# Kernel optimization log

Measured on AMD Instinct MI355X. Metric: run time of the kernel, lower is better.

The kernel has to match this reference:

```python
import jax, jax.numpy as jnp
import numpy as np
from jax import lax

IN_FEATURES = 1024
HIDDEN = 1024
N_LEAVES = 2048
STACK_DEPTH = 4  # comb tree never exceeds stack depth 2


def _make_ops(n_leaves):
    # left-leaning comb tree: shift shift reduce, then (shift reduce)*
    ops = [0, 0, 1] + [0, 1] * (n_leaves - 2)
    return jnp.asarray(np.array(ops, dtype=np.int32))


def _xavier(key, shape):
    fan_in, fan_out = shape[1], shape[0]
    bound = np.sqrt(6.0 / (fan_in + fan_out)).astype(np.float32)
    return jax.random.uniform(key, shape, jnp.float32, -bound, bound)


def setup_inputs() -> dict:
    key = jax.random.key(0)
    k = jax.random.split(key, 4)
    n_nodes = 2 * N_LEAVES - 1
    xs = jax.random.normal(k[0], (n_nodes, IN_FEATURES), jnp.float32)
    ops = _make_ops(N_LEAVES)
    W_ih = _xavier(k[1], (5 * HIDDEN, IN_FEATURES))
    W_lhh = _xavier(k[2], (5 * HIDDEN, HIDDEN))
    W_rhh = _xavier(k[3], (5 * HIDDEN, HIDDEN))
    # biases: zeros except forget-gate slices [H:3H] set to 1 (per reset_parameters)
    b = jnp.zeros((5 * HIDDEN,), jnp.float32).at[HIDDEN:3 * HIDDEN].set(1.0)
    return {"xs": xs, "ops": ops, "W_ih": W_ih, "W_lhh": W_lhh, "W_rhh": W_rhh,
            "b_ih": b, "b_lhh": b, "b_rhh": b}


def _tree_lstm(xs, ops, W_ih, W_lhh, W_rhh, b_ih, b_lhh, b_rhh):
    H = W_lhh.shape[1]
    # hoist the input projection out of the serial scan: [N, 5H]
    ih_all = xs @ W_ih.T + (b_ih + b_lhh + b_rhh)

    def step(carry, inp):
        stack_h, stack_c, ptr = carry  # stack_*: [D, H], ptr: int32 stack size
        ih_t, op = inp
        is_red = op == 1
        ridx = jnp.clip(ptr - 1, 0, STACK_DEPTH - 1)
        lidx = jnp.clip(ptr - 2, 0, STACK_DEPTH - 1)
        zero = jnp.zeros((H,), stack_h.dtype)
        rh = jnp.where(is_red, stack_h[ridx], zero)
        rc = jnp.where(is_red, stack_c[ridx], zero)
        lh = jnp.where(is_red, stack_h[lidx], zero)
        lc = jnp.where(is_red, stack_c[lidx], zero)
        gates = ih_t + lh @ W_lhh.T + rh @ W_rhh.T  # [5H]
        i, lf, rf, g, o = jnp.split(gates, 5)
        i = jax.nn.sigmoid(i)
        lf = jax.nn.sigmoid(lf)
        rf = jax.nn.sigmoid(rf)
        g = jnp.tanh(g)
        o = jax.nn.sigmoid(o)
        yc = lf * lc + rf * rc + i * g
        yh = o * jnp.tanh(yc)
        pos = jnp.where(is_red, ptr - 2, ptr)  # reduce pops 2 then pushes 1
        stack_h = lax.dynamic_update_slice(stack_h, yh[None, :], (pos, 0))
        stack_c = lax.dynamic_update_slice(stack_c, yc[None, :], (pos, 0))
        return (stack_h, stack_c, pos + 1), (yh, yc)

    carry0 = (jnp.zeros((STACK_DEPTH, H), xs.dtype),
              jnp.zeros((STACK_DEPTH, H), xs.dtype),
              jnp.int32(0))
    _, (hs, cs) = lax.scan(step, carry0, (ih_all, ops))
    root_h = hs[-1]  # last produced state is the root (stack ends with size 1)
    return root_h, hs, cs


def reference(xs, ops, W_ih, W_lhh, W_rhh, b_ih, b_lhh, b_rhh):
    return _tree_lstm(xs, ops, W_ih, W_lhh, W_rhh, b_ih, b_lhh, b_rhh)
```

## Files before the change

kernel.cpp:

```cpp
#include <hip/hip_runtime.h>
#include <hip/hip_bf16.h>
#include <stdint.h>

#define HDIM 1024
#define GDIM 5120
#define NWG_SER 128
#define RPW 10
#define NAN_U 0x7FC00000u

typedef __attribute__((ext_vector_type(8))) short v8s;
typedef __attribute__((ext_vector_type(4))) float v4f;

constexpr long long PRE_OFF   = 0;
constexpr long long LEAFG_OFF = PRE_OFF   + 2048LL * 5120 * 4;
constexpr long long DUMP_OFF  = LEAFG_OFF + 2048LL * 5120 * 4;
constexpr long long XSBF_OFF  = DUMP_OFF  + 8192LL * 4;
constexpr long long WIH_OFF   = XSBF_OFF  + 4096LL * 1024 * 2;
constexpr long long WLHH_OFF  = WIH_OFF   + 5120LL * 1024 * 2;
constexpr long long WRHH_OFF  = WLHH_OFF  + 5120LL * 1024 * 2;
constexpr long long HBF_OFF   = WRHH_OFF  + 5120LL * 1024 * 2;
constexpr long long B3_OFF    = HBF_OFF   + 4096LL * 1024 * 2;
constexpr long long PLAN_OFF  = B3_OFF    + 5120LL * 4;

constexpr int P_TRED = 0, P_LNODE = 2048, P_RNODE = 4096, P_FLAGS = 6144,
              P_TLEAF = 8192, P_DEST1 = 10240, P_NODER = 14336, P_DESTR = 16384,
              P_NODEL = 18432, P_DESTL = 20480, P_CNT = 22528;

constexpr int PRE_E   = 0;
constexpr int LEAFG_E = (int)(LEAFG_OFF / 4);
constexpr int DUMP_E  = (int)(DUMP_OFF / 4);

static __device__ __forceinline__ float sigf(float x) { return 1.0f / (1.0f + __expf(-x)); }
static __device__ __forceinline__ float tanh_f(float x) {
  if (x > 15.0f) return 1.0f;
  if (x < -15.0f) return -1.0f;
  float e = __expf(2.0f * x);
  return (e - 1.0f) / (e + 1.0f);
}
static __device__ __forceinline__ unsigned short f2bf(float x) {
  __hip_bfloat16 h = __float2bfloat16(x);
  union { __hip_bfloat16 h; unsigned short u; } cv;
  cv.h = h;
  return cv.u;
}

__global__ void plan_kernel(const int* __restrict__ ops, int n_nodes, int* __restrict__ plan) {
  __shared__ int sops[4096];
  for (int i = threadIdx.x; i < n_nodes; i += 256) sops[i] = ops[i];
  __syncthreads();
  if (threadIdx.x != 0) return;
  int stack[4] = {0, 0, 0, 0};
  int ptr = 0, nred = 0, nleaf = 0, nR = 0, nL = 0;
  for (int t = 0; t < n_nodes; ++t) {
    int op = sops[t];
    if (op == 1) {
      int ridx = min(max(ptr - 1, 0), 3);
      int lidx = min(max(ptr - 2, 0), 3);
      int ln = stack[lidx], rn = stack[ridx];
      int r = nred++;
      plan[P_TRED + r] = t;
      plan[P_LNODE + r] = ln;
      plan[P_RNODE + r] = rn;
      int pos = min(max(ptr - 2, 0), 3);
      int lred = (sops[ln] == 1) ? 1 : 0;
      int rred = (sops[rn] == 1) ? 2 : 0;
      plan[P_FLAGS + r] = lred | rred | (lidx << 2) | (ridx << 4) | (pos << 6);
      plan[P_DEST1 + t] = PRE_E + r * GDIM;
      if (!rred) { plan[P_NODER + nR] = rn; plan[P_DESTR + nR] = PRE_E + r * GDIM; nR++; }
      if (!lred) { plan[P_NODEL + nL] = ln; plan[P_DESTL + nL] = PRE_E + r * GDIM; nL++; }
      stack[pos] = t;
      ptr = (ptr - 2) + 1;
    } else {
      int li = nleaf++;
      plan[P_TLEAF + li] = t;
      plan[P_DEST1 + t] = LEAFG_E + li * GDIM;
      stack[min(max(ptr, 0), 3)] = t;
      ptr = ptr + 1;
    }
  }
  for (int i = n_nodes; i < 4096; ++i) plan[P_DEST1 + i] = DUMP_E;
  for (int i = nR; i < 2048; ++i) { plan[P_NODER + i] = 0; plan[P_DESTR + i] = DUMP_E; }
  for (int i = nL; i < 2048; ++i) { plan[P_NODEL + i] = 0; plan[P_DESTL + i] = DUMP_E; }
  plan[P_CNT + 0] = nred;
  plan[P_CNT + 1] = nR;
  plan[P_CNT + 2] = nL;
  plan[P_CNT + 3] = n_nodes;
}

__global__ void init_nan_kernel(const int* __restrict__ ops, int n_nodes,
                                unsigned int* __restrict__ hsu) {
  const int t = blockIdx.x;
  if (t >= n_nodes || ops[t] != 1) return;
  uint4 nv = make_uint4(NAN_U, NAN_U, NAN_U, NAN_U);
  *(uint4*)(hsu + (long long)t * HDIM + threadIdx.x * 4) = nv;
}

__global__ void cvt_bf16_kernel(const float* __restrict__ src, unsigned short* __restrict__ dst,
                                int ntotal, int nsrc) {
  int i = (blockIdx.x * 256 + threadIdx.x) * 4;
  if (i >= ntotal) return;
  float4 v = make_float4(0.f, 0.f, 0.f, 0.f);
  if (i < nsrc) v = *(const float4*)(src + i);
  ushort4 o;
  o.x = f2bf(v.x); o.y = f2bf(v.y); o.z = f2bf(v.z); o.w = f2bf(v.w);
  *(ushort4*)(dst + i) = o;
}

__global__ void b3_kernel(const float* __restrict__ a, const float* __restrict__ b,
                          const float* __restrict__ c, float* __restrict__ o) {
  int i = blockIdx.x * 256 + threadIdx.x;
  if (i < GDIM) o[i] = a[i] + b[i] + c[i];
}

template <int GATHER, int ACCUM>
__global__ __launch_bounds__(256, 1) void gemm_bt(
    const unsigned short* __restrict__ A, const unsigned short* __restrict__ B,
    const int* __restrict__ gidx, const int* __restrict__ dest,
    float* __restrict__ wsf, const float* __restrict__ b3,
    const int* __restrict__ activeRows) {
  if ((int)blockIdx.x * 128 >= *activeRows) return;
  __shared__ unsigned short As[128 * 32];
  __shared__ unsigned short Bs[128 * 32];
  const int tid = threadIdx.x;
  const int w = tid >> 6, l = tid & 63;
  const int tm = blockIdx.x, tn = blockIdx.y;
  const int q0 = w * 2, q1 = w * 2 + 1;
  const int r0 = q0 * 16 + (l >> 2), r1 = q1 * 16 + (l >> 2);
  const int ck = (l & 3) * 8;
  int ga0 = tm * 128 + r0, ga1 = tm * 128 + r1;
  if (GATHER) { ga0 = gidx[ga0]; ga1 = gidx[ga1]; }
  const unsigned short* ap0 = A + (long long)ga0 * HDIM + ck;
  const unsigned short* ap1 = A + (long long)ga1 * HDIM + ck;
  const unsigned short* bp0 = B + (long long)(tn * 128 + r0) * HDIM + ck;
  const unsigned short* bp1 = B + (long long)(tn * 128 + r1) * HDIM + ck;
  uint4* asd0 = (uint4*)(As + q0 * 512) + l;
  uint4* asd1 = (uint4*)(As + q1 * 512) + l;
  uint4* bsd0 = (uint4*)(Bs + q0 * 512) + l;
  uint4* bsd1 = (uint4*)(Bs + q1 * 512) + l;
  const int wr = w >> 1, wc = w & 1;
  const int lrow = l & 15, lq = l >> 4;
  const unsigned short* Ard = As + (wr * 64 + lrow) * 32 + lq * 8;
  const unsigned short* Brd = Bs + (wc * 64 + lrow) * 32 + lq * 8;
  v4f acc[4][4];
#pragma unroll
  for (int m = 0; m < 4; ++m)
#pragma unroll
    for (int n = 0; n < 4; ++n) acc[m][n] = (v4f){0.f, 0.f, 0.f, 0.f};
  for (int kb = 0; kb < 32; ++kb) {
    const int ko = kb * 32;
    uint4 a0 = *(const uint4*)(ap0 + ko);
    uint4 a1 = *(const uint4*)(ap1 + ko);
    uint4 b0 = *(const uint4*)(bp0 + ko);
    uint4 b1 = *(const uint4*)(bp1 + ko);
    __syncthreads();
    *asd0 = a0; *asd1 = a1; *bsd0 = b0; *bsd1 = b1;
    __syncthreads();
    v8s af[4], bfr[4];
#pragma unroll
    for (int m = 0; m < 4; ++m) af[m] = *(const v8s*)(Ard + m * 512);
#pragma unroll
    for (int n = 0; n < 4; ++n) bfr[n] = *(const v8s*)(Brd + n * 512);
#pragma unroll
    for (int m = 0; m < 4; ++m)
#pragma unroll
      for (int n = 0; n < 4; ++n)
        acc[m][n] = __builtin_amdgcn_mfma_f32_16x16x32_bf16(af[m], bfr[n], acc[m][n], 0, 0, 0);
  }
#pragma unroll
  for (int m = 0; m < 4; ++m) {
#pragma unroll
    for (int jj = 0; jj < 4; ++jj) {
      const int arow = tm * 128 + wr * 64 + m * 16 + lq * 4 + jj;
      const int doff = dest[arow];
#pragma unroll
      for (int n = 0; n < 4; ++n) {
        const int col = tn * 128 + wc * 64 + n * 16 + lrow;
        float v = acc[m][n][jj];
        if (ACCUM) wsf[doff + col] += v;
        else wsf[doff + col] = v + b3[col];
      }
    }
  }
}

__global__ void leaf_cell(const float* __restrict__ leafg, const int* __restrict__ plan,
                          float* __restrict__ hs, float* __restrict__ cs,
                          unsigned short* __restrict__ hbf) {
  const int li = blockIdx.x;
  const int j = threadIdx.x * 4;
  const float* row = leafg + (long long)li * GDIM;
  float4 gi = *(const float4*)(row + j);
  float4 gg = *(const float4*)(row + 3 * HDIM + j);
  float4 go = *(const float4*)(row + 4 * HDIM + j);
  const int t = plan[P_TLEAF + li];
  float4 yc, yh;
  yc.x = sigf(gi.x) * tanh_f(gg.x); yc.y = sigf(gi.y) * tanh_f(gg.y);
  yc.z = sigf(gi.z) * tanh_f(gg.z); yc.w = sigf(gi.w) * tanh_f(gg.w);
  yh.x = sigf(go.x) * tanh_f(yc.x); yh.y = sigf(go.y) * tanh_f(yc.y);
  yh.z = sigf(go.z) * tanh_f(yc.z); yh.w = sigf(go.w) * tanh_f(yc.w);
  *(float4*)(hs + (long long)t * HDIM + j) = yh;
  *(float4*)(cs + (long long)t * HDIM + j) = yc;
  ushort4 hb;
  hb.x = f2bf(yh.x); hb.y = f2bf(yh.y); hb.z = f2bf(yh.z); hb.w = f2bf(yh.w);
  *(ushort4*)(hbf + (long long)t * HDIM + j) = hb;
}

__global__ __launch_bounds__(256, 1) void serial_chain(
    const float* __restrict__ Wl, const float* __restrict__ Wr,
    const float* __restrict__ pre, const int* __restrict__ plan,
    float* __restrict__ hs, float* __restrict__ cs) {
  const int wg = blockIdx.x;
  const int tid = threadIdx.x;
  const int w = tid >> 6, l = tid & 63;
  __shared__ int s_t[2048], s_ln[2048], s_rn[2048], s_fl[2048];
  __shared__ float gsum[40];
  __shared__ float c_stack[4][8];
  const int nred = plan[P_CNT + 0];
  for (int i = tid; i < nred; i += 256) {
    s_t[i] = plan[P_TRED + i];
    s_ln[i] = plan[P_LNODE + i];
    s_rn[i] = plan[P_RNODE + i];
    s_fl[i] = plan[P_FLAGS + i];
  }
  float wreg[RPW][16];
#pragma unroll
  for (int rr = 0; rr < RPW; ++rr) {
    const int ridx = w * RPW + rr;
    const long long row = (long long)((ridx >> 3) * HDIM + wg * 8 + (ridx & 7)) * HDIM;
#pragma unroll
    for (int q = 0; q < 16; ++q) wreg[rr][q] = Wl[row + q * 64 + l];
  }
  float pv0 = 0.f, pv1 = 0.f, pv2 = 0.f, pv3 = 0.f, pv4 = 0.f;
  if (tid < 8) {
    const float* pr = pre + wg * 8 + tid;
    pv0 = pr[0]; pv1 = pr[HDIM]; pv2 = pr[2 * HDIM]; pv3 = pr[3 * HDIM]; pv4 = pr[4 * HDIM];
  }
  __syncthreads();
  for (int r = 0; r < nred; ++r) {
    const int t = s_t[r], ln = s_ln[r], rn = s_rn[r], fl = s_fl[r];
    float lc = 0.f, rc = 0.f;
    if (tid < 8) {
      const int jj = wg * 8 + tid;
      if (fl & 1) lc = c_stack[(fl >> 2) & 3][tid];
      else        lc = cs[(long long)ln * HDIM + jj];
      if (fl & 2) rc = c_stack[(fl >> 4) & 3][tid];
      else        rc = cs[(long long)rn * HDIM + jj];
    }
    float hv[16];
    {
      const float* hrow = hs + (long long)ln * HDIM;
      if (fl & 1) {
        bool ready = false;
        while (!ready) {
          ready = true;
#pragma unroll
          for (int q = 0; q < 16; ++q) {
            unsigned int u = __hip_atomic_load((unsigned int*)(hrow + q * 64 + l),
                                               __ATOMIC_RELAXED, __HIP_MEMORY_SCOPE_AGENT);
            ready = ready && (u != NAN_U);
            hv[q] = __uint_as_float(u);
          }
        }
      } else {
#pragma unroll
        for (int q = 0; q < 16; ++q) hv[q] = hrow[q * 64 + l];
      }
    }
    float acc[RPW];
#pragma unroll
    for (int rr = 0; rr < RPW; ++rr) acc[rr] = 0.f;
#pragma unroll
    for (int rr = 0; rr < RPW; ++rr)
#pragma unroll
      for (int q = 0; q < 16; ++q) acc[rr] = fmaf(wreg[rr][q], hv[q], acc[rr]);
    if (fl & 2) {
      float hv2[16];
      const float* hrow2 = hs + (long long)rn * HDIM;
      bool ready = false;
      while (!ready) {
        ready = true;
#pragma unroll
        for (int q = 0; q < 16; ++q) {
          unsigned int u = __hip_atomic_load((unsigned int*)(hrow2 + q * 64 + l),
                                             __ATOMIC_RELAXED, __HIP_MEMORY_SCOPE_AGENT);
          ready = ready && (u != NAN_U);
          hv2[q] = __uint_as_float(u);
        }
      }
#pragma unroll
      for (int rr = 0; rr < RPW; ++rr) {
        const int ridx = w * RPW + rr;
        const long long row = (long long)((ridx >> 3) * HDIM + wg * 8 + (ridx & 7)) * HDIM;
#pragma unroll
        for (int q = 0; q < 16; ++q) acc[rr] = fmaf(Wr[row + q * 64 + l], hv2[q], acc[rr]);
      }
    }
#pragma unroll
    for (int rr = 0; rr < RPW; ++rr) {
      float v = acc[rr];
      v += __shfl_xor(v, 32); v += __shfl_xor(v, 16); v += __shfl_xor(v, 8);
      v += __shfl_xor(v, 4);  v += __shfl_xor(v, 2);  v += __shfl_xor(v, 1);
      if (l == 0) gsum[w * RPW + rr] = v;
    }
    __syncthreads();
    if (tid < 8) {
      const int jj = wg * 8 + tid;
      const float xi  = pv0 + gsum[0 * 8 + tid];
      const float xlf = pv1 + gsum[1 * 8 + tid];
      const float xrf = pv2 + gsum[2 * 8 + tid];
      const float xg  = pv3 + gsum[3 * 8 + tid];
      const float xo  = pv4 + gsum[4 * 8 + tid];
      const float ii = sigf(xi), lf = sigf(xlf), rf = sigf(xrf);
      const float gv = tanh_f(xg), oo = sigf(xo);
      const float yc = lf * lc + rf * rc + ii * gv;
      const float yh = oo * tanh_f(yc);
      cs[(long long)t * HDIM + jj] = yc;
      c_stack[(fl >> 6) & 3][tid] = yc;
      __hip_atomic_store((unsigned int*)&hs[(long long)t * HDIM + jj], __float_as_uint(yh),
                         __ATOMIC_RELAXED, __HIP_MEMORY_SCOPE_AGENT);
      if (r + 1 < nred) {
        const float* pr = pre + (long long)(r + 1) * GDIM + jj;
        pv0 = pr[0]; pv1 = pr[HDIM]; pv2 = pr[2 * HDIM]; pv3 = pr[3 * HDIM]; pv4 = pr[4 * HDIM];
      }
    }
    __syncthreads();
  }
}

__global__ void root_copy(float* __restrict__ out, const float* __restrict__ hs, int n_nodes) {
  int j = blockIdx.x * 256 + threadIdx.x;
  if (j < HDIM) out[j] = hs[(long long)(n_nodes - 1) * HDIM + j];
}

extern "C" void kernel_launch(void* const* d_in, const int* in_sizes, int n_in,
                              void* d_out, int out_size, void* d_ws, size_t ws_size,
                              hipStream_t stream) {
  const float* xs = (const float*)d_in[0];
  const int* ops = (const int*)d_in[1];
  const float* Wih = (const float*)d_in[2];
  const float* Wlhh = (const float*)d_in[3];
  const float* Wrhh = (const float*)d_in[4];
  const float* bih = (const float*)d_in[5];
  const float* blhh = (const float*)d_in[6];
  const float* brhh = (const float*)d_in[7];
  const int n_nodes = in_sizes[0] / HDIM;

  char* ws = (char*)d_ws;
  float* wsf = (float*)d_ws;
  float* pre = (float*)(ws + PRE_OFF);
  float* leafg = (float*)(ws + LEAFG_OFF);
  unsigned short* xsbf = (unsigned short*)(ws + XSBF_OFF);
  unsigned short* wihb = (unsigned short*)(ws + WIH_OFF);
  unsigned short* wlhb = (unsigned short*)(ws + WLHH_OFF);
  unsigned short* wrhb = (unsigned short*)(ws + WRHH_OFF);
  unsigned short* hbf = (unsigned short*)(ws + HBF_OFF);
  float* b3 = (float*)(ws + B3_OFF);
  int* plan = (int*)(ws + PLAN_OFF);

  float* out = (float*)d_out;
  float* hs = out + HDIM;
  float* cs = hs + (long long)n_nodes * HDIM;

  hipLaunchKernelGGL(plan_kernel, dim3(1), dim3(256), 0, stream, ops, n_nodes, plan);
  hipLaunchKernelGGL(init_nan_kernel, dim3(n_nodes), dim3(256), 0, stream,
                     ops, n_nodes, (unsigned int*)hs);
  hipLaunchKernelGGL(cvt_bf16_kernel, dim3(4096), dim3(256), 0, stream,
                     xs, xsbf, 4096 * HDIM, n_nodes * HDIM);
  hipLaunchKernelGGL(cvt_bf16_kernel, dim3(5120), dim3(256), 0, stream,
                     Wih, wihb, GDIM * HDIM, GDIM * HDIM);
  hipLaunchKernelGGL(cvt_bf16_kernel, dim3(5120), dim3(256), 0, stream,
                     Wlhh, wlhb, GDIM * HDIM, GDIM * HDIM);
  hipLaunchKernelGGL(cvt_bf16_kernel, dim3(5120), dim3(256), 0, stream,
                     Wrhh, wrhb, GDIM * HDIM, GDIM * HDIM);
  hipLaunchKernelGGL(b3_kernel, dim3(20), dim3(256), 0, stream, bih, blhh, brhh, b3);
  hipLaunchKernelGGL((gemm_bt<0, 0>), dim3(32, 40), dim3(256), 0, stream,
                     xsbf, wihb, (const int*)nullptr, plan + P_DEST1, wsf, b3, plan + P_CNT + 3);
  hipLaunchKernelGGL(leaf_cell, dim3((n_nodes + 1) / 2), dim3(256), 0, stream,
                     leafg, plan, hs, cs, hbf);
  hipLaunchKernelGGL((gemm_bt<1, 1>), dim3(16, 40), dim3(256), 0, stream,
                     hbf, wrhb, plan + P_NODER, plan + P_DESTR, wsf, (const float*)nullptr, plan + P_CNT + 1);
  hipLaunchKernelGGL((gemm_bt<1, 1>), dim3(16, 40), dim3(256), 0, stream,
                     hbf, wlhb, plan + P_NODEL, plan + P_DESTL, wsf, (const float*)nullptr, plan + P_CNT + 2);
  hipLaunchKernelGGL(serial_chain, dim3(NWG_SER), dim3(256), 0, stream,
                     Wlhh, Wrhh, pre, plan, hs, cs);
  hipLaunchKernelGGL(root_copy, dim3(4), dim3(256), 0, stream, out, hs, n_nodes);
}
```

Measured before the change: 9.616 ms.

## Halve serial-chain workgroups and stage polled h vectors in LDS

The serial recurrence kernel now runs 64 workgroups of 512 threads, each covering 16 hidden units instead of 8. That halves the number of workgroups polling global memory for each new hidden state. Polling is also reduced: only one wavefront polls the left child's h and another polls the right child's, using 64-bit atomic loads, and they share the values through LDS with an extra barrier. This cuts redundant cross-workgroup spin traffic at the cost of an added __syncthreads per step and more register pressure from the launch bound of 2.

```diff
diff --git a/kernel.cpp b/kernel.cpp
--- a/kernel.cpp
+++ b/kernel.cpp
@@ -4,7 +4,8 @@
 
 #define HDIM 1024
 #define GDIM 5120
-#define NWG_SER 128
+#define NWG_SER 64
+#define TPB_SER 512
 #define RPW 10
 #define NAN_U 0x7FC00000u
 
@@ -205,7 +206,7 @@
   *(ushort4*)(hbf + (long long)t * HDIM + j) = hb;
 }
 
-__global__ __launch_bounds__(256, 1) void serial_chain(
+__global__ __launch_bounds__(TPB_SER, 2) void serial_chain(
     const float* __restrict__ Wl, const float* __restrict__ Wr,
     const float* __restrict__ pre, const int* __restrict__ plan,
     float* __restrict__ hs, float* __restrict__ cs) {
@@ -213,10 +214,12 @@
   const int tid = threadIdx.x;
   const int w = tid >> 6, l = tid & 63;
   __shared__ int s_t[2048], s_ln[2048], s_rn[2048], s_fl[2048];
-  __shared__ float gsum[40];
-  __shared__ float c_stack[4][8];
+  __shared__ float h_sh[1024];
+  __shared__ float h_sh2[1024];
+  __shared__ float gsum[80];
+  __shared__ float c_stack[4][16];
   const int nred = plan[P_CNT + 0];
-  for (int i = tid; i < nred; i += 256) {
+  for (int i = tid; i < nred; i += TPB_SER) {
     s_t[i] = plan[P_TRED + i];
     s_ln[i] = plan[P_LNODE + i];
     s_rn[i] = plan[P_RNODE + i];
@@ -226,46 +229,77 @@
 #pragma unroll
   for (int rr = 0; rr < RPW; ++rr) {
     const int ridx = w * RPW + rr;
-    const long long row = (long long)((ridx >> 3) * HDIM + wg * 8 + (ridx & 7)) * HDIM;
+    const long long row = (long long)((ridx >> 4) * HDIM + wg * 16 + (ridx & 15)) * HDIM;
 #pragma unroll
     for (int q = 0; q < 16; ++q) wreg[rr][q] = Wl[row + q * 64 + l];
   }
   float pv0 = 0.f, pv1 = 0.f, pv2 = 0.f, pv3 = 0.f, pv4 = 0.f;
-  if (tid < 8) {
-    const float* pr = pre + wg * 8 + tid;
+  if (tid < 16) {
+    const float* pr = pre + wg * 16 + tid;
     pv0 = pr[0]; pv1 = pr[HDIM]; pv2 = pr[2 * HDIM]; pv3 = pr[3 * HDIM]; pv4 = pr[4 * HDIM];
   }
   __syncthreads();
   for (int r = 0; r < nred; ++r) {
     const int t = s_t[r], ln = s_ln[r], rn = s_rn[r], fl = s_fl[r];
     float lc = 0.f, rc = 0.f;
-    if (tid < 8) {
-      const int jj = wg * 8 + tid;
+    if (tid < 16) {
+      const int jj = wg * 16 + tid;
       if (fl & 1) lc = c_stack[(fl >> 2) & 3][tid];
       else        lc = cs[(long long)ln * HDIM + jj];
       if (fl & 2) rc = c_stack[(fl >> 4) & 3][tid];
       else        rc = cs[(long long)rn * HDIM + jj];
     }
-    float hv[16];
-    {
-      const float* hrow = hs + (long long)ln * HDIM;
+    if (w == 0) {
+      const unsigned long long* hrow = (const unsigned long long*)(hs + (long long)ln * HDIM);
+      unsigned long long hv64[8];
       if (fl & 1) {
         bool ready = false;
         while (!ready) {
           ready = true;
 #pragma unroll
-          for (int q = 0; q < 16; ++q) {
-            unsigned int u = __hip_atomic_load((unsigned int*)(hrow + q * 64 + l),
-                                               __ATOMIC_RELAXED, __HIP_MEMORY_SCOPE_AGENT);
-            ready = ready && (u != NAN_U);
-            hv[q] = __uint_as_float(u);
+          for (int p = 0; p < 8; ++p) {
+            unsigned long long u = __hip_atomic_load(hrow + p * 64 + l,
+                                                     __ATOMIC_RELAXED, __HIP_MEMORY_SCOPE_AGENT);
+            ready = ready && ((unsigned int)u != NAN_U) && ((unsigned int)(u >> 32) != NAN_U);
+            hv64[p] = u;
           }
         }
       } else {
 #pragma unroll
-        for (int q = 0; q < 16; ++q) hv[q] = hrow[q * 64 + l];
-      }
-    }
+        for (int p = 0; p < 8; ++p) hv64[p] = hrow[p * 64 + l];
+      }
+#pragma unroll
+      for (int p = 0; p < 8; ++p) {
+        const int c = (p * 64 + l) * 2;
+        h_sh[c] = __uint_as_float((unsigned int)hv64[p]);
+        h_sh[c + 1] = __uint_as_float((unsigned int)(hv64[p] >> 32));
+      }
+    }
+    if ((fl & 2) && w == 1) {
+      const unsigned long long* hrow = (const unsigned long long*)(hs + (long long)rn * HDIM);
+      unsigned long long hv64[8];
+      bool ready = false;
+      while (!ready) {
+        ready = true;
+#pragma unroll
+        for (int p = 0; p < 8; ++p) {
+          unsigned long long u = __hip_atomic_load(hrow + p * 64 + l,
+                                                   __ATOMIC_RELAXED, __HIP_MEMORY_SCOPE_AGENT);
+          ready = ready && ((unsigned int)u != NAN_U) && ((unsigned int)(u >> 32) != NAN_U);
+          hv64[p] = u;
+        }
+      }
+#pragma unroll
+      for (int p = 0; p < 8; ++p) {
+        const int c = (p * 64 + l) * 2;
+        h_sh2[c] = __uint_as_float((unsigned int)hv64[p]);
+        h_sh2[c + 1] = __uint_as_float((unsigned int)(hv64[p] >> 32));
+      }
+    }
+    __syncthreads();
+    float hv[16];
+#pragma unroll
+    for (int q = 0; q < 16; ++q) hv[q] = h_sh[q * 64 + l];
     float acc[RPW];
 #pragma unroll
     for (int rr = 0; rr < RPW; ++rr) acc[rr] = 0.f;
@@ -275,22 +309,12 @@
       for (int q = 0; q < 16; ++q) acc[rr] = fmaf(wreg[rr][q], hv[q], acc[rr]);
     if (fl & 2) {
       float hv2[16];
-      const float* hrow2 = hs + (long long)rn * HDIM;
-      bool ready = false;
-      while (!ready) {
-        ready = true;
-#pragma unroll
-        for (int q = 0; q < 16; ++q) {
-          unsigned int u = __hip_atomic_load((unsigned int*)(hrow2 + q * 64 + l),
-                                             __ATOMIC_RELAXED, __HIP_MEMORY_SCOPE_AGENT);
-          ready = ready && (u != NAN_U);
-          hv2[q] = __uint_as_float(u);
-        }
-      }
+#pragma unroll
+      for (int q = 0; q < 16; ++q) hv2[q] = h_sh2[q * 64 + l];
 #pragma unroll
       for (int rr = 0; rr < RPW; ++rr) {
         const int ridx = w * RPW + rr;
-        const long long row = (long long)((ridx >> 3) * HDIM + wg * 8 + (ridx & 7)) * HDIM;
+        const long long row = (long long)((ridx >> 4) * HDIM + wg * 16 + (ridx & 15)) * HDIM;
 #pragma unroll
         for (int q = 0; q < 16; ++q) acc[rr] = fmaf(Wr[row + q * 64 + l], hv2[q], acc[rr]);
       }
@@ -303,13 +327,13 @@
       if (l == 0) gsum[w * RPW + rr] = v;
     }
     __syncthreads();
-    if (tid < 8) {
-      const int jj = wg * 8 + tid;
-      const float xi  = pv0 + gsum[0 * 8 + tid];
-      const float xlf = pv1 + gsum[1 * 8 + tid];
-      const float xrf = pv2 + gsum[2 * 8 + tid];
-      const float xg  = pv3 + gsum[3 * 8 + tid];
-      const float xo  = pv4 + gsum[4 * 8 + tid];
+    if (tid < 16) {
+      const int jj = wg * 16 + tid;
+      const float xi  = pv0 + gsum[0 * 16 + tid];
+      const float xlf = pv1 + gsum[1 * 16 + tid];
+      const float xrf = pv2 + gsum[2 * 16 + tid];
+      const float xg  = pv3 + gsum[3 * 16 + tid];
+      const float xo  = pv4 + gsum[4 * 16 + tid];
       const float ii = sigf(xi), lf = sigf(xlf), rf = sigf(xrf);
       const float gv = tanh_f(xg), oo = sigf(xo);
       const float yc = lf * lc + rf * rc + ii * gv;
@@ -381,7 +405,7 @@
                      hbf, wrhb, plan + P_NODER, plan + P_DESTR, wsf, (const float*)nullptr, plan + P_CNT + 1);
   hipLaunchKernelGGL((gemm_bt<1, 1>), dim3(16, 40), dim3(256), 0, stream,
                      hbf, wlhb, plan + P_NODEL, plan + P_DESTL, wsf, (const float*)nullptr, plan + P_CNT + 2);
-  hipLaunchKernelGGL(serial_chain, dim3(NWG_SER), dim3(256), 0, stream,
+  hipLaunchKernelGGL(serial_chain, dim3(NWG_SER), dim3(TPB_SER), 0, stream,
                      Wlhh, Wrhh, pre, plan, hs, cs);
   hipLaunchKernelGGL(root_copy, dim3(4), dim3(256), 0, stream, out, hs, n_nodes);
 }
```

New measurement: 11.57 ms. 1.2x slower.

## Make serial chain waves independent with per-wave channel ownership and ready flags

Applied to the files above, without the earlier changes.

Each wave in the serial recurrence kernel now owns two hidden channels and computes all five gates for them. The gate reduction and cell update stay inside the wave, which removes the two block-wide barriers and the LDS gate exchange on every step. A per-wave byte-flag window in workspace is polled before the NaN-sentinel check on dependent hidden rows, with s_sleep backoff in the spin loops. In exchange the flags are never reset, so they only gate correctly within the first window and otherwise rely on the NaN polling. Each wave also re-reads Wr rows directly and issues more small global loads per step.

```diff
diff --git a/kernel.cpp b/kernel.cpp
--- a/kernel.cpp
+++ b/kernel.cpp
@@ -5,8 +5,9 @@
 #define HDIM 1024
 #define GDIM 5120
 #define NWG_SER 128
-#define RPW 10
+#define TPB_SER 256
 #define NAN_U 0x7FC00000u
+#define FLAG_WIN 64
 
 typedef __attribute__((ext_vector_type(8))) short v8s;
 typedef __attribute__((ext_vector_type(4))) float v4f;
@@ -21,10 +22,12 @@
 constexpr long long HBF_OFF   = WRHH_OFF  + 5120LL * 1024 * 2;
 constexpr long long B3_OFF    = HBF_OFF   + 4096LL * 1024 * 2;
 constexpr long long PLAN_OFF  = B3_OFF    + 5120LL * 4;
+constexpr long long FLAG_OFF  = PLAN_OFF  + 26688LL * 4;
 
 constexpr int P_TRED = 0, P_LNODE = 2048, P_RNODE = 4096, P_FLAGS = 6144,
               P_TLEAF = 8192, P_DEST1 = 10240, P_NODER = 14336, P_DESTR = 16384,
-              P_NODEL = 18432, P_DESTL = 20480, P_CNT = 22528;
+              P_NODEL = 18432, P_DESTL = 20480, P_CNT = 22528,
+              P_LRX = 22592, P_RRX = 24640;
 
 constexpr int PRE_E   = 0;
 constexpr int LEAFG_E = (int)(LEAFG_OFF / 4);
@@ -46,6 +49,7 @@
 
 __global__ void plan_kernel(const int* __restrict__ ops, int n_nodes, int* __restrict__ plan) {
   __shared__ int sops[4096];
+  __shared__ int red_of[4096];
   for (int i = threadIdx.x; i < n_nodes; i += 256) sops[i] = ops[i];
   __syncthreads();
   if (threadIdx.x != 0) return;
@@ -65,9 +69,12 @@
       int lred = (sops[ln] == 1) ? 1 : 0;
       int rred = (sops[rn] == 1) ? 2 : 0;
       plan[P_FLAGS + r] = lred | rred | (lidx << 2) | (ridx << 4) | (pos << 6);
+      plan[P_LRX + r] = lred ? red_of[ln] : 0;
+      plan[P_RRX + r] = rred ? red_of[rn] : 0;
       plan[P_DEST1 + t] = PRE_E + r * GDIM;
       if (!rred) { plan[P_NODER + nR] = rn; plan[P_DESTR + nR] = PRE_E + r * GDIM; nR++; }
       if (!lred) { plan[P_NODEL + nL] = ln; plan[P_DESTL + nL] = PRE_E + r * GDIM; nL++; }
+      red_of[t] = r;
       stack[pos] = t;
       ptr = (ptr - 2) + 1;
     } else {
@@ -205,125 +212,163 @@
   *(ushort4*)(hbf + (long long)t * HDIM + j) = hb;
 }
 
-__global__ __launch_bounds__(256, 1) void serial_chain(
+__global__ __launch_bounds__(TPB_SER, 1) void serial_chain(
     const float* __restrict__ Wl, const float* __restrict__ Wr,
     const float* __restrict__ pre, const int* __restrict__ plan,
-    float* __restrict__ hs, float* __restrict__ cs) {
+    float* __restrict__ hs, float* __restrict__ cs,
+    unsigned char* __restrict__ flags) {
   const int wg = blockIdx.x;
   const int tid = threadIdx.x;
   const int w = tid >> 6, l = tid & 63;
-  __shared__ int s_t[2048], s_ln[2048], s_rn[2048], s_fl[2048];
-  __shared__ float gsum[40];
-  __shared__ float c_stack[4][8];
+  const int wid = wg * 4 + w;
+  const int ch0 = wid * 2;
+  __shared__ int s_t[2048], s_ln[2048], s_rn[2048], s_fl[2048], s_lrx[2048], s_rrx[2048];
   const int nred = plan[P_CNT + 0];
-  for (int i = tid; i < nred; i += 256) {
+  for (int i = tid; i < nred; i += TPB_SER) {
     s_t[i] = plan[P_TRED + i];
     s_ln[i] = plan[P_LNODE + i];
     s_rn[i] = plan[P_RNODE + i];
     s_fl[i] = plan[P_FLAGS + i];
+    s_lrx[i] = plan[P_LRX + i];
+    s_rrx[i] = plan[P_RRX + i];
   }
-  float wreg[RPW][16];
-#pragma unroll
-  for (int rr = 0; rr < RPW; ++rr) {
-    const int ridx = w * RPW + rr;
-    const long long row = (long long)((ridx >> 3) * HDIM + wg * 8 + (ridx & 7)) * HDIM;
-#pragma unroll
-    for (int q = 0; q < 16; ++q) wreg[rr][q] = Wl[row + q * 64 + l];
-  }
-  float pv0 = 0.f, pv1 = 0.f, pv2 = 0.f, pv3 = 0.f, pv4 = 0.f;
-  if (tid < 8) {
-    const float* pr = pre + wg * 8 + tid;
-    pv0 = pr[0]; pv1 = pr[HDIM]; pv2 = pr[2 * HDIM]; pv3 = pr[3 * HDIM]; pv4 = pr[4 * HDIM];
-  }
+  float wreg[10][16];
+#pragma unroll
+  for (int c = 0; c < 2; ++c)
+#pragma unroll
+    for (int g = 0; g < 5; ++g) {
+      const float* wp = Wl + (long long)(g * HDIM + ch0 + c) * HDIM + l;
+#pragma unroll
+      for (int q = 0; q < 16; ++q) wreg[c * 5 + g][q] = wp[q * 64];
+    }
+  float cst0 = 0.f, cst1 = 0.f, cst2 = 0.f, cst3 = 0.f;
   __syncthreads();
+  unsigned int* fu = (unsigned int*)flags;
   for (int r = 0; r < nred; ++r) {
     const int t = s_t[r], ln = s_ln[r], rn = s_rn[r], fl = s_fl[r];
-    float lc = 0.f, rc = 0.f;
-    if (tid < 8) {
-      const int jj = wg * 8 + tid;
-      if (fl & 1) lc = c_stack[(fl >> 2) & 3][tid];
-      else        lc = cs[(long long)ln * HDIM + jj];
-      if (fl & 2) rc = c_stack[(fl >> 4) & 3][tid];
-      else        rc = cs[(long long)rn * HDIM + jj];
+    float pv0 = 0.f, pv1 = 0.f, pv2 = 0.f, pv3 = 0.f, pv4 = 0.f, lcv = 0.f, rcv = 0.f;
+    if (l < 2) {
+      const float* pr = pre + (long long)r * GDIM + ch0 + l;
+      pv0 = pr[0]; pv1 = pr[HDIM]; pv2 = pr[2 * HDIM]; pv3 = pr[3 * HDIM]; pv4 = pr[4 * HDIM];
+      if (!(fl & 1)) lcv = cs[(long long)ln * HDIM + ch0 + l];
+      if (!(fl & 2)) rcv = cs[(long long)rn * HDIM + ch0 + l];
+    }
+    {
+      const int lidx = (fl >> 2) & 3, ridx = (fl >> 4) & 3;
+      const float lst = (lidx == 0) ? cst0 : (lidx == 1) ? cst1 : (lidx == 2) ? cst2 : cst3;
+      const float rst = (ridx == 0) ? cst0 : (ridx == 1) ? cst1 : (ridx == 2) ? cst2 : cst3;
+      if (fl & 1) lcv = lst;
+      if (fl & 2) rcv = rst;
+    }
+    if (fl & 1) {
+      const unsigned int* fwp = fu + (unsigned)((s_lrx[r] & (FLAG_WIN - 1)) * 128);
+      for (;;) {
+        unsigned int d0 = __hip_atomic_load(fwp + l, __ATOMIC_RELAXED, __HIP_MEMORY_SCOPE_AGENT);
+        unsigned int d1 = __hip_atomic_load(fwp + 64 + l, __ATOMIC_RELAXED, __HIP_MEMORY_SCOPE_AGENT);
+        if (__all((d0 == 0x01010101u) && (d1 == 0x01010101u))) break;
+        __builtin_amdgcn_s_sleep(1);
+      }
     }
     float hv[16];
     {
       const float* hrow = hs + (long long)ln * HDIM;
       if (fl & 1) {
-        bool ready = false;
-        while (!ready) {
-          ready = true;
+        for (;;) {
+          bool ready = true;
 #pragma unroll
           for (int q = 0; q < 16; ++q) {
-            unsigned int u = __hip_atomic_load((unsigned int*)(hrow + q * 64 + l),
+            unsigned int u = __hip_atomic_load((const unsigned int*)(hrow + q * 64 + l),
                                                __ATOMIC_RELAXED, __HIP_MEMORY_SCOPE_AGENT);
             ready = ready && (u != NAN_U);
             hv[q] = __uint_as_float(u);
           }
+          if (__all(ready)) break;
+          __builtin_amdgcn_s_sleep(1);
         }
       } else {
 #pragma unroll
         for (int q = 0; q < 16; ++q) hv[q] = hrow[q * 64 + l];
       }
     }
-    float acc[RPW];
-#pragma unroll
-    for (int rr = 0; rr < RPW; ++rr) acc[rr] = 0.f;
-#pragma unroll
-    for (int rr = 0; rr < RPW; ++rr)
-#pragma unroll
-      for (int q = 0; q < 16; ++q) acc[rr] = fmaf(wreg[rr][q], hv[q], acc[rr]);
+    float acc[10];
+#pragma unroll
+    for (int k = 0; k < 10; ++k) acc[k] = 0.f;
+#pragma unroll
+    for (int k = 0; k < 10; ++k)
+#pragma unroll
+      for (int q = 0; q < 16; ++q) acc[k] = fmaf(wreg[k][q], hv[q], acc[k]);
     if (fl & 2) {
+      const unsigned int* fwp = fu + (unsigned)((s_rrx[r] & (FLAG_WIN - 1)) * 128);
+      for (;;) {
+        unsigned int d0 = __hip_atomic_load(fwp + l, __ATOMIC_RELAXED, __HIP_MEMORY_SCOPE_AGENT);
+        unsigned int d1 = __hip_atomic_load(fwp + 64 + l, __ATOMIC_RELAXED, __HIP_MEMORY_SCOPE_AGENT);
+        if (__all((d0 == 0x01010101u) && (d1 == 0x01010101u))) break;
+        __builtin_amdgcn_s_sleep(1);
+      }
       float hv2[16];
       const float* hrow2 = hs + (long long)rn * HDIM;
-      bool ready = false;
-      while (!ready) {
-        ready = true;
+      for (;;) {
+        bool ready = true;
 #pragma unroll
         for (int q = 0; q < 16; ++q) {
-          unsigned int u = __hip_atomic_load((unsigned int*)(hrow2 + q * 64 + l),
+          unsigned int u = __hip_atomic_load((const unsigned int*)(hrow2 + q * 64 + l),
                                              __ATOMIC_RELAXED, __HIP_MEMORY_SCOPE_AGENT);
           ready = ready && (u != NAN_U);
           hv2[q] = __uint_as_float(u);
         }
+        if (__all(ready)) break;
+        __builtin_amdgcn_s_sleep(1);
       }
 #pragma unroll
-      for (int rr = 0; rr < RPW; ++rr) {
-        const int ridx = w * RPW + rr;
-        const long long row = (long long)((ridx >> 3) * HDIM + wg * 8 + (ridx & 7)) * HDIM;
-#pragma unroll
-        for (int q = 0; q < 16; ++q) acc[rr] = fmaf(Wr[row + q * 64 + l], hv2[q], acc[rr]);
-      }
-    }
-#pragma unroll
-    for (int rr = 0; rr < RPW; ++rr) {
-      float v = acc[rr];
+      for (int c = 0; c < 2; ++c)
+#pragma unroll
+        for (int g = 0; g < 5; ++g) {
+          const float* wp = Wr + (long long)(g * HDIM + ch0 + c) * HDIM + l;
+#pragma unroll
+          for (int q = 0; q < 16; ++q) acc[c * 5 + g] = fmaf(wp[q * 64], hv2[q], acc[c * 5 + g]);
+        }
+    }
+#pragma unroll
+    for (int k = 0; k < 10; ++k) {
+      float v = acc[k];
       v += __shfl_xor(v, 32); v += __shfl_xor(v, 16); v += __shfl_xor(v, 8);
       v += __shfl_xor(v, 4);  v += __shfl_xor(v, 2);  v += __shfl_xor(v, 1);
-      if (l == 0) gsum[w * RPW + rr] = v;
-    }
-    __syncthreads();
-    if (tid < 8) {
-      const int jj = wg * 8 + tid;
-      const float xi  = pv0 + gsum[0 * 8 + tid];
-      const float xlf = pv1 + gsum[1 * 8 + tid];
-      const float xrf = pv2 + gsum[2 * 8 + tid];
-      const float xg  = pv3 + gsum[3 * 8 + tid];
-      const float xo  = pv4 + gsum[4 * 8 + tid];
-      const float ii = sigf(xi), lf = sigf(xlf), rf = sigf(xrf);
-      const float gv = tanh_f(xg), oo = sigf(xo);
-      const float yc = lf * lc + rf * rc + ii * gv;
-      const float yh = oo * tanh_f(yc);
-      cs[(long long)t * HDIM + jj] = yc;
-      c_stack[(fl >> 6) & 3][tid] = yc;
-      __hip_atomic_store((unsigned int*)&hs[(long long)t * HDIM + jj], __float_as_uint(yh),
+      acc[k] = v;
+    }
+    float yh_l = 0.f, yc_l = 0.f;
+    if (l < 2) {
+      const float ai  = (l == 0) ? acc[0] : acc[5];
+      const float alf = (l == 0) ? acc[1] : acc[6];
+      const float arf = (l == 0) ? acc[2] : acc[7];
+      const float ag  = (l == 0) ? acc[3] : acc[8];
+      const float ao  = (l == 0) ? acc[4] : acc[9];
+      const float ii = sigf(pv0 + ai), lf = sigf(pv1 + alf), rf = sigf(pv2 + arf);
+      const float gv = tanh_f(pv3 + ag), oo = sigf(pv4 + ao);
+      yc_l = lf * lcv + rf * rcv + ii * gv;
+      yh_l = oo * tanh_f(yc_l);
+    }
+    {
+      const int pos = (fl >> 6) & 3;
+      cst0 = (pos == 0) ? yc_l : cst0;
+      cst1 = (pos == 1) ? yc_l : cst1;
+      cst2 = (pos == 2) ? yc_l : cst2;
+      cst3 = (pos == 3) ? yc_l : cst3;
+    }
+    const float yh1 = __shfl(yh_l, 1);
+    const float yc1 = __shfl(yc_l, 1);
+    if (l == 0) {
+      float2 c2; c2.x = yc_l; c2.y = yc1;
+      *(float2*)(cs + (long long)t * HDIM + ch0) = c2;
+      unsigned long long pk = ((unsigned long long)__float_as_uint(yh1) << 32) |
+                              (unsigned long long)__float_as_uint(yh_l);
+      __hip_atomic_store((unsigned long long*)(hs + (long long)t * HDIM + ch0), pk,
                          __ATOMIC_RELAXED, __HIP_MEMORY_SCOPE_AGENT);
-      if (r + 1 < nred) {
-        const float* pr = pre + (long long)(r + 1) * GDIM + jj;
-        pv0 = pr[0]; pv1 = pr[HDIM]; pv2 = pr[2 * HDIM]; pv3 = pr[3 * HDIM]; pv4 = pr[4 * HDIM];
-      }
-    }
-    __syncthreads();
+    }
+    __asm__ volatile("s_waitcnt vmcnt(0)" ::: "memory");
+    if (l == 0) {
+      __hip_atomic_store(flags + (unsigned)((r & (FLAG_WIN - 1)) * 512 + wid),
+                         (unsigned char)1, __ATOMIC_RELAXED, __HIP_MEMORY_SCOPE_AGENT);
+    }
   }
 }
 
@@ -356,6 +401,7 @@
   unsigned short* hbf = (unsigned short*)(ws + HBF_OFF);
   float* b3 = (float*)(ws + B3_OFF);
   int* plan = (int*)(ws + PLAN_OFF);
+  unsigned char* flags = (unsigned char*)(ws + FLAG_OFF);
 
   float* out = (float*)d_out;
   float* hs = out + HDIM;
@@ -381,7 +427,7 @@
                      hbf, wrhb, plan + P_NODER, plan + P_DESTR, wsf, (const float*)nullptr, plan + P_CNT + 1);
   hipLaunchKernelGGL((gemm_bt<1, 1>), dim3(16, 40), dim3(256), 0, stream,
                      hbf, wlhb, plan + P_NODEL, plan + P_DESTL, wsf, (const float*)nullptr, plan + P_CNT + 2);
-  hipLaunchKernelGGL(serial_chain, dim3(NWG_SER), dim3(256), 0, stream,
-                     Wlhh, Wrhh, pre, plan, hs, cs);
+  hipLaunchKernelGGL(serial_chain, dim3(NWG_SER), dim3(TPB_SER), 0, stream,
+                     Wlhh, Wrhh, pre, plan, hs, cs, flags);
   hipLaunchKernelGGL(root_copy, dim3(4), dim3(256), 0, stream, out, hs, n_nodes);
 }
```

Result: slower. 16.25 ms (+69.0%).
